# Optimization experiments

Measured on AMD Instinct MI355X. Metric: run time of the kernel, lower is better.

## Reference

```python
import jax, jax.numpy as jnp
import numpy as np

B, N, D = 4, 4096, 256
EPS = 1e-5


def setup_inputs() -> dict:
    key = jax.random.key(0)
    ks = jax.random.split(key, 6)
    x = jax.random.normal(ks[0], (B, N, D), dtype=jnp.float32)
    coord = jax.random.normal(ks[1], (B, N, D), dtype=jnp.float32)
    ln_g = jnp.ones((D,), dtype=jnp.float32)
    ln_b = jnp.zeros((D,), dtype=jnp.float32)
    s = 1.0 / np.sqrt(D)
    w_qkv = jax.random.normal(ks[2], (D, 3 * D), dtype=jnp.float32) * s
    w_out = jax.random.normal(ks[3], (D, D), dtype=jnp.float32) * s
    b_out = jnp.zeros((D,), dtype=jnp.float32)
    return {"x": x, "coord": coord, "ln_g": ln_g, "ln_b": ln_b,
            "w_qkv": w_qkv, "w_out": w_out, "b_out": b_out}


def reference(x, coord, ln_g, ln_b, w_qkv, w_out, b_out):
    d = x.shape[-1]
    scale = d ** (-0.5)
    # LayerNorm over last dim
    mu = jnp.mean(x, axis=-1, keepdims=True)
    var = jnp.var(x, axis=-1, keepdims=True)
    nx = (x - mu) * jax.lax.rsqrt(var + EPS) * ln_g + ln_b
    # QKV projection (no bias), chunk into q,k,v
    qkv = jnp.einsum('bnd,de->bne', nx, w_qkv)
    q, k, v = jnp.split(qkv, 3, axis=-1)
    # coord bias on q and k (module does NOT split into heads)
    q = q + coord
    k = k + coord
    dots = jnp.einsum('bnd,bmd->bnm', q, k) * scale
    attn = jax.nn.softmax(dots, axis=-1)
    out = jnp.einsum('bnm,bmd->bnd', attn, v)
    return jnp.einsum('bnd,de->bne', out, w_out) + b_out
```

## Files before the change

### kernel.cpp

```cpp
#include <hip/hip_runtime.h>
#include <hip/hip_fp16.h>
#include <math.h>

constexpr int B = 4, N = 4096, D = 256;
constexpr int BN = B * N;
constexpr float EPS = 1e-5f;
constexpr float QSC2 = 0.0625f * 1.44269504088896340736f;

constexpr int SPLIT = 4;
constexpr int KVB = 32;
constexpr int NTK = (N / SPLIT) / KVB;
constexpr float THR = 8.0f;

typedef __attribute__((ext_vector_type(8))) _Float16 f16x8;
typedef __attribute__((ext_vector_type(2))) __fp16 fp16x2;
typedef __attribute__((ext_vector_type(4))) float f32x4;
typedef __attribute__((ext_vector_type(16))) float f32x16;

__device__ inline f32x4 mfma_f16(f16x8 a, f16x8 b, f32x4 c) {
  return __builtin_amdgcn_mfma_f32_16x16x32_f16(a, b, c, 0, 0, 0);
}
__device__ inline f32x16 mfma32(f16x8 a, f16x8 b, f32x16 c) {
  return __builtin_amdgcn_mfma_f32_32x32x16_f16(a, b, c, 0, 0, 0);
}
__device__ inline ushort f2h(float x) {
  __half h = __float2half(x);
  return *(ushort*)&h;
}
__device__ inline float h2f(ushort u) {
  __half h;
  *(ushort*)&h = u;
  return __half2float(h);
}
__device__ inline unsigned pkh(float a, float b) {
  fp16x2 r = __builtin_amdgcn_cvt_pkrtz(a, b);
  return *(unsigned*)&r;
}
__device__ inline void gload16(const ushort* g, ushort* l) {
  __builtin_amdgcn_global_load_lds(
      (const __attribute__((address_space(1))) void*)g,
      (__attribute__((address_space(3))) void*)l, 16, 0, 0);
}

__global__ __launch_bounds__(256) void ln_kernel(
    const float* __restrict__ x, const float* __restrict__ g,
    const float* __restrict__ bta, ushort* __restrict__ nxh) {
  const int row = blockIdx.x;
  const int t = threadIdx.x;
  const float v = x[(size_t)row * D + t];
  float s = v, ss = v * v;
#pragma unroll
  for (int o = 32; o > 0; o >>= 1) {
    s += __shfl_down(s, o);
    ss += __shfl_down(ss, o);
  }
  __shared__ float red[8];
  if ((t & 63) == 0) {
    red[t >> 6] = s;
    red[(t >> 6) + 4] = ss;
  }
  __syncthreads();
  s = red[0] + red[1] + red[2] + red[3];
  ss = red[4] + red[5] + red[6] + red[7];
  const float mu = s * (1.0f / D);
  const float var = ss * (1.0f / D) - mu * mu;
  const float rsig = rsqrtf(var + EPS);
  const float nx = (v - mu) * rsig * g[t] + bta[t];
  nxh[(size_t)row * D + t] = f2h(nx);
}

__global__ __launch_bounds__(256) void castw_kernel(
    const float* __restrict__ w_qkv, const float* __restrict__ w_out,
    ushort* __restrict__ wt, ushort* __restrict__ wot) {
  const int id = blockIdx.x * 256 + threadIdx.x;
  if (id < 768 * 256) {
    const int n = id >> 8, k = id & 255;
    wt[id] = f2h(w_qkv[(size_t)k * 768 + n]);
  } else {
    const int j = id - 768 * 256;
    const int n = j >> 8, k = j & 255;
    wot[j] = f2h(w_out[(size_t)k * 256 + n]);
  }
}

__global__ __launch_bounds__(256, 4) void qkv_kernel(
    const ushort* __restrict__ nxh, const ushort* __restrict__ wt,
    const float* __restrict__ coord, ushort* __restrict__ qfp,
    ushort* __restrict__ kfp, ushort* __restrict__ vtp) {
  const int t = threadIdx.x;
  const int w = t >> 6, lane = t & 63;
  const int lrow = lane & 15, lhi = lane >> 4;
  const int m0 = blockIdx.x * 128 + w * 32;
  const int c0 = blockIdx.y * 64;
  f32x4 acc[2][4];
#pragma unroll
  for (int qs = 0; qs < 2; ++qs)
#pragma unroll
    for (int nt = 0; nt < 4; ++nt) acc[qs][nt] = f32x4{0.f, 0.f, 0.f, 0.f};

#pragma unroll
  for (int kc = 0; kc < D; kc += 32) {
    f16x8 ah[2], bw[4];
#pragma unroll
    for (int qs = 0; qs < 2; ++qs)
      ah[qs] = *(const f16x8*)(nxh + (size_t)(m0 + qs * 16 + lrow) * D + kc +
                               lhi * 8);
#pragma unroll
    for (int nt = 0; nt < 4; ++nt)
      bw[nt] = *(const f16x8*)(wt + (size_t)(c0 + nt * 16 + lrow) * D + kc +
                               lhi * 8);
#pragma unroll
    for (int qs = 0; qs < 2; ++qs)
#pragma unroll
      for (int nt = 0; nt < 4; ++nt)
        acc[qs][nt] = mfma_f16(ah[qs], bw[nt], acc[qs][nt]);
  }

  const int region = blockIdx.y >> 2;
  const int cbase = c0 & 255;
  if (region < 2) {
    const float sc = (region == 0) ? QSC2 : 1.0f;
    ushort* dp = (region == 0) ? qfp : kfp;
#pragma unroll
    for (int qs = 0; qs < 2; ++qs)
#pragma unroll
      for (int nt = 0; nt < 4; ++nt)
#pragma unroll
        for (int i = 0; i < 4; ++i) {
          const int row = m0 + qs * 16 + lhi * 4 + i;
          const int col = cbase + nt * 16 + lrow;
          const float val =
              (acc[qs][nt][i] + coord[(size_t)row * D + col]) * sc;
          dp[(size_t)row * D + col] = f2h(val);
        }
  } else {
#pragma unroll
    for (int qs = 0; qs < 2; ++qs)
#pragma unroll
      for (int nt = 0; nt < 4; ++nt)
#pragma unroll
        for (int i = 0; i < 4; ++i) {
          const int row = m0 + qs * 16 + lhi * 4 + i;
          const int col = cbase + nt * 16 + lrow;
          const int bb = row >> 12, n = row & (N - 1);
          vtp[((size_t)bb * D + col) * N + n] = f2h(acc[qs][nt][i]);
        }
  }
}

__global__ __launch_bounds__(512, 2) void attn_kernel(
    const ushort* __restrict__ qf, const ushort* __restrict__ kf,
    const ushort* __restrict__ vt, ushort* __restrict__ pob,
    float* __restrict__ mlb) {
  __shared__ ushort kbuf[4][8192];
  __shared__ ushort vbuf[4][8192];

  const int tid = threadIdx.x;
  const int lane = tid & 63;
  const int q = lane & 31, h = lane >> 5;
  const int w = tid >> 6;
  const int b = blockIdx.y, s = blockIdx.z;
  const int qw = blockIdx.x * 256 + w * 32;
  const int kbeg = s * (N / SPLIT);

  const ushort* qrow = qf + ((size_t)b * N + qw + q) * D;
  const ushort* kfb = kf + (size_t)b * N * D;
  const ushort* vtb = vt + (size_t)b * D * N;
  ushort* pog = pob + (size_t)s * BN * D;
  float* mlg = mlb + (size_t)s * BN * 2;

  f16x8 qfr[8];
#pragma unroll
  for (int c = 0; c < 8; ++c)
    qfr[c] = *(const f16x8*)(qrow + c * 16 + h * 8);

  f32x16 o[8];
#pragma unroll
  for (int dt = 0; dt < 8; ++dt)
#pragma unroll
    for (int r = 0; r < 16; ++r) o[dt][r] = 0.f;
  float m = -1e30f, lsum = 0.f;
  float f_prev = 1.0f;
  bool need_prev = false;
  f16x8 pf_prev[2];

  auto stage = [&](int bi, int k0) {
#pragma unroll
    for (int i = 0; i < 2; ++i) {
      const int g = i * 512 + tid;
      const int key = g >> 5, slot = g & 31;
      gload16(kfb + (size_t)(k0 + key) * D + ((slot ^ (key & 7)) * 8),
              &kbuf[bi][g * 8]);
    }
#pragma unroll
    for (int i = 0; i < 2; ++i) {
      const int g = i * 512 + tid;
      const int r = g >> 3, slot = g & 7;
      const int u = slot ^ (r & 7);
      const int d = r * 2 + (u >> 2);
      gload16(vtb + (size_t)d * N + k0 + ((u & 3) * 8), &vbuf[bi][g * 8]);
    }
  };

  stage(0, kbeg);

  for (int t = 0; t < NTK; ++t) {
    const int cur = t & 3;
    const int prv = (t + 3) & 3;
    f16x8 qs[8];
#pragma unroll
    for (int c = 0; c < 8; ++c)
      qs[c] = *(const f16x8*)(qrow + (8 + c) * 16 + h * 8);
    if (t + 1 < NTK) {
      stage((t + 1) & 3, kbeg + (t + 1) * KVB);
      asm volatile("s_waitcnt vmcnt(12)" ::: "memory");
    } else {
      asm volatile("s_waitcnt vmcnt(8)" ::: "memory");
    }
    __builtin_amdgcn_sched_barrier(0);
    __builtin_amdgcn_s_barrier();
    __builtin_amdgcn_sched_barrier(0);

    f32x16 p;
#pragma unroll
    for (int r = 0; r < 16; ++r) p[r] = 0.f;
    const int ksw = (q & 7);
    __builtin_amdgcn_s_setprio(1);
#pragma unroll
    for (int c = 0; c < 16; ++c) {
      const f16x8 qv = (c < 8) ? qfr[c] : qs[c - 8];
      const f16x8 ka = *(const f16x8*)&kbuf[cur][q * 256 +
                                                 (((c * 2 + h) ^ ksw) * 8)];
      p = mfma32(ka, qv, p);
    }
    __builtin_amdgcn_s_setprio(0);

    if (t > 0) {
      if (need_prev) {
#pragma unroll
        for (int dt = 0; dt < 8; ++dt) o[dt] *= f_prev;
      }
      __builtin_amdgcn_s_setprio(1);
#pragma unroll
      for (int dt = 0; dt < 8; ++dt) {
        const int d = dt * 32 + q;
        const int rr = d >> 1;
#pragma unroll
        for (int kk = 0; kk < 2; ++kk) {
          const int u = (d & 1) * 4 + kk * 2 + h;
          const f16x8 vf = *(const f16x8*)&vbuf[prv][rr * 64 +
                                                     ((u ^ (rr & 7)) * 8)];
          o[dt] = mfma32(vf, pf_prev[kk], o[dt]);
        }
      }
      __builtin_amdgcn_s_setprio(0);
    }

    float tm[8];
#pragma unroll
    for (int j = 0; j < 8; ++j) tm[j] = fmaxf(p[2 * j], p[2 * j + 1]);
    float pmax = fmaxf(fmaxf(fmaxf(tm[0], tm[1]), fmaxf(tm[2], tm[3])),
                       fmaxf(fmaxf(tm[4], tm[5]), fmaxf(tm[6], tm[7])));
    const float pm = fmaxf(pmax, __shfl_xor(pmax, 32));
    const bool need = pm > m + THR;
    if (__any(need)) {
      const float mn = fmaxf(m, pm);
      f_prev = exp2f(m - mn);
      m = mn;
      lsum *= f_prev;
      need_prev = true;
    } else {
      need_prev = false;
    }
#pragma unroll
    for (int r = 0; r < 16; ++r) {
      p[r] = exp2f(p[r] - m);
      lsum += p[r];
    }

#pragma unroll
    for (int kk = 0; kk < 2; ++kk) {
      const int sub = kk * 8;
      unsigned x = pkh(p[sub + 0], p[sub + 1]);
      unsigned z = pkh(p[sub + 2], p[sub + 3]);
      unsigned y = pkh(p[sub + 4], p[sub + 5]);
      unsigned wv = pkh(p[sub + 6], p[sub + 7]);
      const unsigned xs = __shfl_xor(x, 32);
      const unsigned zs = __shfl_xor(z, 32);
      const unsigned ys = __shfl_xor(y, 32);
      const unsigned ws = __shfl_xor(wv, 32);
      union { f16x8 v; unsigned u[4]; } pu;
      pu.u[0] = h ? ys : x;
      pu.u[1] = h ? ws : z;
      pu.u[2] = h ? y : xs;
      pu.u[3] = h ? wv : zs;
      pf_prev[kk] = pu.v;
    }
  }

  if (need_prev) {
#pragma unroll
    for (int dt = 0; dt < 8; ++dt) o[dt] *= f_prev;
  }
  {
    const int prv = (NTK - 1) & 3;
#pragma unroll
    for (int dt = 0; dt < 8; ++dt) {
      const int d = dt * 32 + q;
      const int rr = d >> 1;
#pragma unroll
      for (int kk = 0; kk < 2; ++kk) {
        const int u = (d & 1) * 4 + kk * 2 + h;
        const f16x8 vf = *(const f16x8*)&vbuf[prv][rr * 64 +
                                                   ((u ^ (rr & 7)) * 8)];
        o[dt] = mfma32(vf, pf_prev[kk], o[dt]);
      }
    }
  }
  const float lt = lsum + __shfl_xor(lsum, 32);
  const float inv = 1.0f / lt;
  ushort* orow = pog + ((size_t)b * N + qw + q) * D;
#pragma unroll
  for (int dt = 0; dt < 8; ++dt)
#pragma unroll
    for (int r4 = 0; r4 < 4; ++r4) {
      const unsigned u0 =
          pkh(o[dt][r4 * 4 + 0] * inv, o[dt][r4 * 4 + 1] * inv);
      const unsigned u1 =
          pkh(o[dt][r4 * 4 + 2] * inv, o[dt][r4 * 4 + 3] * inv);
      uint2 val;
      val.x = u0;
      val.y = u1;
      *(uint2*)(orow + dt * 32 + r4 * 8 + h * 4) = val;
    }
  if (h == 0) {
    const size_t r = (size_t)b * N + qw + q;
    mlg[r * 2] = m;
    mlg[r * 2 + 1] = lt;
  }
}

__global__ __launch_bounds__(256, 4) void projm_kernel(
    const ushort* __restrict__ pob, const float* __restrict__ mlb,
    const ushort* __restrict__ wot, const float* __restrict__ bias,
    float* __restrict__ out) {
  const int t = threadIdx.x;
  const int w = t >> 6, lane = t & 63;
  const int lrow = lane & 15, lhi = lane >> 4;
  const int m0 = blockIdx.x * 128 + w * 32;
  const int c0 = blockIdx.y * 64;

  float cw[2][SPLIT];
#pragma unroll
  for (int qs = 0; qs < 2; ++qs) {
    const int row = m0 + qs * 16 + lrow;
    float mv[SPLIT], lv[SPLIT], mm = -1e30f;
#pragma unroll
    for (int s = 0; s < SPLIT; ++s) {
      mv[s] = mlb[(size_t)s * BN * 2 + row * 2];
      lv[s] = mlb[(size_t)s * BN * 2 + row * 2 + 1];
      mm = fmaxf(mm, mv[s]);
    }
    float wsum = 0.f;
#pragma unroll
    for (int s = 0; s < SPLIT; ++s) {
      cw[qs][s] = exp2f(mv[s] - mm) * lv[s];
      wsum += cw[qs][s];
    }
    const float invw = 1.0f / wsum;
#pragma unroll
    for (int s = 0; s < SPLIT; ++s) cw[qs][s] *= invw;
  }

  f32x4 acc[2][4];
#pragma unroll
  for (int qs = 0; qs < 2; ++qs)
#pragma unroll
    for (int nt = 0; nt < 4; ++nt) acc[qs][nt] = f32x4{0.f, 0.f, 0.f, 0.f};

#pragma unroll
  for (int kc = 0; kc < D; kc += 32) {
    f16x8 ah[2], bw[4];
#pragma unroll
    for (int qs = 0; qs < 2; ++qs) {
      const size_t off = (size_t)(m0 + qs * 16 + lrow) * D + kc + lhi * 8;
      float v[8] = {};
#pragma unroll
      for (int s = 0; s < SPLIT; ++s) {
        const f16x8 ps = *(const f16x8*)(pob + (size_t)s * BN * D + off);
        const float c = cw[qs][s];
#pragma unroll
        for (int j = 0; j < 8; ++j) v[j] += c * (float)ps[j];
      }
      f16x8 a;
#pragma unroll
      for (int j = 0; j < 8; ++j) a[j] = (_Float16)v[j];
      ah[qs] = a;
    }
#pragma unroll
    for (int nt = 0; nt < 4; ++nt)
      bw[nt] = *(const f16x8*)(wot + (size_t)(c0 + nt * 16 + lrow) * D + kc +
                               lhi * 8);
#pragma unroll
    for (int qs = 0; qs < 2; ++qs)
#pragma unroll
      for (int nt = 0; nt < 4; ++nt)
        acc[qs][nt] = mfma_f16(ah[qs], bw[nt], acc[qs][nt]);
  }
#pragma unroll
  for (int qs = 0; qs < 2; ++qs)
#pragma unroll
    for (int nt = 0; nt < 4; ++nt)
#pragma unroll
      for (int i = 0; i < 4; ++i) {
        const int row = m0 + qs * 16 + lhi * 4 + i;
        const int col = c0 + nt * 16 + lrow;
        out[(size_t)row * D + col] = acc[qs][nt][i] + bias[col];
      }
}

extern "C" void kernel_launch(void* const* d_in, const int* in_sizes, int n_in,
                              void* d_out, int out_size, void* d_ws, size_t ws_size,
                              hipStream_t stream) {
  const float* x = (const float*)d_in[0];
  const float* coord = (const float*)d_in[1];
  const float* ln_g = (const float*)d_in[2];
  const float* ln_b = (const float*)d_in[3];
  const float* w_qkv = (const float*)d_in[4];
  const float* w_out = (const float*)d_in[5];
  const float* b_out = (const float*)d_in[6];
  float* out = (float*)d_out;

  const size_t P = (size_t)BN * D;

  ushort* qfp = (ushort*)d_ws;
  ushort* kfp = qfp + P;
  ushort* vtp = kfp + P;
  ushort* pob = vtp + P;
  float* mlb = (float*)(pob + (size_t)SPLIT * P);
  ushort* wt = (ushort*)(mlb + (size_t)SPLIT * BN * 2);
  ushort* wot = wt + 768 * 256;
  ushort* nxh = pob;

  hipLaunchKernelGGL(ln_kernel, dim3(BN), dim3(256), 0, stream,
                     x, ln_g, ln_b, nxh);
  hipLaunchKernelGGL(castw_kernel, dim3(1024), dim3(256), 0, stream,
                     w_qkv, w_out, wt, wot);
  hipLaunchKernelGGL(qkv_kernel, dim3(BN / 128, 12), dim3(256), 0, stream,
                     nxh, wt, coord, qfp, kfp, vtp);
  hipLaunchKernelGGL(attn_kernel, dim3(N / 256, B, SPLIT), dim3(512), 0,
                     stream, qfp, kfp, vtp, pob, mlb);
  hipLaunchKernelGGL(projm_kernel, dim3(BN / 128, 4), dim3(256), 0, stream,
                     pob, mlb, wot, b_out, out);
}
```

Baseline: 185.1 us.

## Fuse layernorm with weight cast and stage V transpose through LDS

Merges the layernorm and weight-cast kernels into one launch. The layernorm now handles 8 rows per block, with a half-wave per row, vectorized float4 loads, f16x8 stores and xor shuffles in place of LDS reductions. The V-transpose store in the QKV kernel now goes through a padded shared-memory tile, so global writes are contiguous 8-byte runs along N instead of scattered 2-byte stores. This removes one launch and uncoalesced transposed writes, at the cost of extra LDS and a barrier in the V-region blocks.

```diff
diff --git a/kernel.cpp b/kernel.cpp
--- a/kernel.cpp
+++ b/kernel.cpp
@@ -42,44 +42,52 @@
       (__attribute__((address_space(3))) void*)l, 16, 0, 0);
 }
 
-__global__ __launch_bounds__(256) void ln_kernel(
+__global__ __launch_bounds__(256) void lncast_kernel(
     const float* __restrict__ x, const float* __restrict__ g,
-    const float* __restrict__ bta, ushort* __restrict__ nxh) {
-  const int row = blockIdx.x;
-  const int t = threadIdx.x;
-  const float v = x[(size_t)row * D + t];
-  float s = v, ss = v * v;
-#pragma unroll
-  for (int o = 32; o > 0; o >>= 1) {
-    s += __shfl_down(s, o);
-    ss += __shfl_down(ss, o);
-  }
-  __shared__ float red[8];
-  if ((t & 63) == 0) {
-    red[t >> 6] = s;
-    red[(t >> 6) + 4] = ss;
-  }
-  __syncthreads();
-  s = red[0] + red[1] + red[2] + red[3];
-  ss = red[4] + red[5] + red[6] + red[7];
-  const float mu = s * (1.0f / D);
-  const float var = ss * (1.0f / D) - mu * mu;
-  const float rsig = rsqrtf(var + EPS);
-  const float nx = (v - mu) * rsig * g[t] + bta[t];
-  nxh[(size_t)row * D + t] = f2h(nx);
-}
-
-__global__ __launch_bounds__(256) void castw_kernel(
+    const float* __restrict__ bta, ushort* __restrict__ nxh,
     const float* __restrict__ w_qkv, const float* __restrict__ w_out,
     ushort* __restrict__ wt, ushort* __restrict__ wot) {
-  const int id = blockIdx.x * 256 + threadIdx.x;
-  if (id < 768 * 256) {
-    const int n = id >> 8, k = id & 255;
-    wt[id] = f2h(w_qkv[(size_t)k * 768 + n]);
-  } else {
-    const int j = id - 768 * 256;
-    const int n = j >> 8, k = j & 255;
-    wot[j] = f2h(w_out[(size_t)k * 256 + n]);
+  const int tid = threadIdx.x;
+  const int lane = tid & 63;
+  const int row = blockIdx.x * 8 + (tid >> 6) * 2 + (lane >> 5);
+  const int e0 = (lane & 31) * 8;
+  const float4 a = *(const float4*)&x[(size_t)row * D + e0];
+  const float4 bv = *(const float4*)&x[(size_t)row * D + e0 + 4];
+  float s = a.x + a.y + a.z + a.w + bv.x + bv.y + bv.z + bv.w;
+  float ss = a.x * a.x + a.y * a.y + a.z * a.z + a.w * a.w +
+             bv.x * bv.x + bv.y * bv.y + bv.z * bv.z + bv.w * bv.w;
+#pragma unroll
+  for (int off = 1; off < 32; off <<= 1) {
+    s += __shfl_xor(s, off);
+    ss += __shfl_xor(ss, off);
+  }
+  const float mu = s * (1.0f / D);
+  const float rsig = rsqrtf(ss * (1.0f / D) - mu * mu + EPS);
+  const float4 g0 = *(const float4*)&g[e0];
+  const float4 g1 = *(const float4*)&g[e0 + 4];
+  const float4 b0 = *(const float4*)&bta[e0];
+  const float4 b1 = *(const float4*)&bta[e0 + 4];
+  f16x8 r;
+  r[0] = (_Float16)((a.x - mu) * rsig * g0.x + b0.x);
+  r[1] = (_Float16)((a.y - mu) * rsig * g0.y + b0.y);
+  r[2] = (_Float16)((a.z - mu) * rsig * g0.z + b0.z);
+  r[3] = (_Float16)((a.w - mu) * rsig * g0.w + b0.w);
+  r[4] = (_Float16)((bv.x - mu) * rsig * g1.x + b1.x);
+  r[5] = (_Float16)((bv.y - mu) * rsig * g1.y + b1.y);
+  r[6] = (_Float16)((bv.z - mu) * rsig * g1.z + b1.z);
+  r[7] = (_Float16)((bv.w - mu) * rsig * g1.w + b1.w);
+  *(f16x8*)&nxh[(size_t)row * D + e0] = r;
+
+  if (blockIdx.x < 1024) {
+    const int id = blockIdx.x * 256 + tid;
+    if (id < 768 * 256) {
+      const int n = id >> 8, k = id & 255;
+      wt[id] = f2h(w_qkv[(size_t)k * 768 + n]);
+    } else {
+      const int j = id - 768 * 256;
+      const int n = j >> 8, k = j & 255;
+      wot[j] = f2h(w_out[(size_t)k * 256 + n]);
+    }
   }
 }
 
@@ -87,6 +95,7 @@
     const ushort* __restrict__ nxh, const ushort* __restrict__ wt,
     const float* __restrict__ coord, ushort* __restrict__ qfp,
     ushort* __restrict__ kfp, ushort* __restrict__ vtp) {
+  __shared__ ushort vs[64 * 132];
   const int t = threadIdx.x;
   const int w = t >> 6, lane = t & 63;
   const int lrow = lane & 15, lhi = lane >> 4;
@@ -137,14 +146,24 @@
 #pragma unroll
     for (int qs = 0; qs < 2; ++qs)
 #pragma unroll
-      for (int nt = 0; nt < 4; ++nt)
-#pragma unroll
-        for (int i = 0; i < 4; ++i) {
-          const int row = m0 + qs * 16 + lhi * 4 + i;
-          const int col = cbase + nt * 16 + lrow;
-          const int bb = row >> 12, n = row & (N - 1);
-          vtp[((size_t)bb * D + col) * N + n] = f2h(acc[qs][nt][i]);
-        }
+      for (int nt = 0; nt < 4; ++nt) {
+        ushort4 pk;
+        pk.x = f2h(acc[qs][nt][0]);
+        pk.y = f2h(acc[qs][nt][1]);
+        pk.z = f2h(acc[qs][nt][2]);
+        pk.w = f2h(acc[qs][nt][3]);
+        *(ushort4*)&vs[(nt * 16 + lrow) * 132 + w * 32 + qs * 16 + lhi * 4] =
+            pk;
+      }
+    __syncthreads();
+    const int c = t >> 2, seg = (t & 3) * 32;
+    const int nb0 = blockIdx.x * 128;
+    const int bb = nb0 >> 12, nb = nb0 & (N - 1);
+    ushort* dst = vtp + ((size_t)bb * D + cbase + c) * N + nb + seg;
+    const ushort* src = &vs[c * 132 + seg];
+#pragma unroll
+    for (int k2 = 0; k2 < 8; ++k2)
+      *(uint2*)(dst + k2 * 4) = *(const uint2*)(src + k2 * 4);
   }
 }
 
@@ -442,10 +461,8 @@
   ushort* wot = wt + 768 * 256;
   ushort* nxh = pob;
 
-  hipLaunchKernelGGL(ln_kernel, dim3(BN), dim3(256), 0, stream,
-                     x, ln_g, ln_b, nxh);
-  hipLaunchKernelGGL(castw_kernel, dim3(1024), dim3(256), 0, stream,
-                     w_qkv, w_out, wt, wot);
+  hipLaunchKernelGGL(lncast_kernel, dim3(BN / 8), dim3(256), 0, stream,
+                     x, ln_g, ln_b, nxh, w_qkv, w_out, wt, wot);
   hipLaunchKernelGGL(qkv_kernel, dim3(BN / 128, 12), dim3(256), 0, stream,
                      nxh, wt, coord, qfp, kfp, vtp);
   hipLaunchKernelGGL(attn_kernel, dim3(N / 256, B, SPLIT), dim3(512), 0,
```

Result: faster. 174.3 us (-5.8%).
